# Optimization experiments

Hardware: AMD Instinct MI355X
Metric: run time of the kernel (lower is better)

Reference implementation:

```python
import jax, jax.numpy as jnp
import numpy as np

N, E, B = 50000, 800000, 64
D_IN, D_E = 192, 64
NUM_OUT = 256


def setup_inputs() -> dict:
    key = jax.random.key(0)
    ks = jax.random.split(key, 30)
    rn = lambda k, s: jax.random.normal(k, s, dtype=jnp.float32) * 0.05
    return {
        "x": jax.random.normal(ks[0], (N, D_IN), jnp.float32),
        "edge_index": jax.random.randint(ks[1], (2, E), 0, N, dtype=jnp.int32),
        "edge_attr": jax.random.normal(ks[2], (E, D_E), jnp.float32),
        "batch": jnp.sort(jax.random.randint(ks[3], (N,), 0, B, dtype=jnp.int32)),
        "W1": rn(ks[4], (D_IN, 256)), "as1": rn(ks[5], (4, 64)), "ad1": rn(ks[6], (4, 64)),
        "We1": rn(ks[7], (D_E, 256)), "ae1": rn(ks[8], (4, 64)), "b1": rn(ks[9], (256,)),
        "W2": rn(ks[10], (256, 256)), "as2": rn(ks[11], (4, 64)), "ad2": rn(ks[12], (4, 64)),
        "We2": rn(ks[13], (D_E, 256)), "ae2": rn(ks[14], (4, 64)), "b2": rn(ks[15], (256,)),
        "W3": rn(ks[16], (256, 512)), "as3": rn(ks[17], (4, 128)), "ad3": rn(ks[18], (4, 128)),
        "We3": rn(ks[19], (D_E, 512)), "ae3": rn(ks[20], (4, 128)), "b3": rn(ks[21], (128,)),
        "Wa": rn(ks[22], (128, NUM_OUT)), "ba": rn(ks[23], (NUM_OUT,)),
        "Wv": rn(ks[24], (128, 1)), "bv": rn(ks[25], (1,)),
    }


def reference(x, edge_index, edge_attr, batch,
              W1, as1, ad1, We1, ae1, b1,
              W2, as2, ad2, We2, ae2, b2,
              W3, as3, ad3, We3, ae3, b3,
              Wa, ba, Wv, bv):
    Nn = x.shape[0]
    src0, dst0 = edge_index[0], edge_index[1]
    # PyG add_self_loops(fill_value='mean'): self-loop edge_attr = mean of incoming edge_attr
    deg = jax.ops.segment_sum(jnp.ones_like(dst0, dtype=x.dtype), dst0, num_segments=Nn)
    loop_attr = jax.ops.segment_sum(edge_attr, dst0, num_segments=Nn) / jnp.maximum(deg, 1.0)[:, None]
    loop = jnp.arange(Nn, dtype=src0.dtype)
    src = jnp.concatenate([src0, loop])
    dst = jnp.concatenate([dst0, loop])
    ea = jnp.concatenate([edge_attr, loop_attr], axis=0)

    def gat(h, W, a_s, a_d, We, a_e, bias, concat):
        Hh, C = a_s.shape
        hs = (h @ W).reshape(Nn, Hh, C)                       # [N,H,C]
        al_s = (hs * a_s).sum(-1)                             # [N,H]
        al_d = (hs * a_d).sum(-1)                             # [N,H]
        al_e = ((ea @ We).reshape(-1, Hh, C) * a_e).sum(-1)   # [E+N,H]
        alpha = jax.nn.leaky_relu(al_s[src] + al_d[dst] + al_e, 0.2)
        amax = jax.ops.segment_max(alpha, dst, num_segments=Nn)
        w = jnp.exp(alpha - amax[dst])
        denom = jax.ops.segment_sum(w, dst, num_segments=Nn)
        w = w / (denom[dst] + 1e-16)                          # scatter-softmax over dst
        out = jax.ops.segment_sum(hs[src] * w[..., None], dst, num_segments=Nn)
        out = out.reshape(Nn, Hh * C) if concat else out.mean(axis=1)
        return out + bias

    h = jax.nn.relu(gat(x, W1, as1, ad1, We1, ae1, b1, True))
    h = jax.nn.relu(gat(h, W2, as2, ad2, We2, ae2, b2, True))
    h = gat(h, W3, as3, ad3, We3, ae3, b3, False)
    cnt = jax.ops.segment_sum(jnp.ones((Nn,), h.dtype), batch, num_segments=B)
    g = jax.ops.segment_sum(h, batch, num_segments=B) / jnp.maximum(cnt, 1.0)[:, None]
    logits = g @ Wa + ba
    value = g @ Wv + bv
    return jnp.concatenate([logits, value], axis=-1)  # [B, num_outputs+1]
```

## Files before the change

kernel.cpp:

```cpp
#include <hip/hip_runtime.h>
#include <hip/hip_bf16.h>


typedef __attribute__((ext_vector_type(8))) short short8;
typedef __attribute__((ext_vector_type(4))) float floatx4;

#define DEV __device__ __forceinline__

DEV unsigned short f2b(float f) {
  union { float f; unsigned u; } v; v.f = f;
  unsigned r = v.u + 0x7FFFu + ((v.u >> 16) & 1u);
  return (unsigned short)(r >> 16);
}
DEV float b2f(unsigned short u) {
  union { unsigned u; float f; } v; v.u = ((unsigned)u) << 16;
  return v.f;
}

__global__ void k_deg(const int* __restrict__ dst, int* __restrict__ deg, int E) {
  int e = blockIdx.x * 256 + threadIdx.x;
  if (e < E) atomicAdd(&deg[dst[e]], 1);
}

__global__ __launch_bounds__(1024) void k_scan(const int* __restrict__ deg,
    int* __restrict__ rowptr, int* __restrict__ cursor, int N, int E) {
  __shared__ int sd[1024];
  __shared__ int s_carry;
  int tid = threadIdx.x;
  if (tid == 0) s_carry = 0;
  __syncthreads();
  for (int base = 0; base < N; base += 8192) {
    int i0 = base + tid * 8;
    int v[8]; int s = 0;
#pragma unroll
    for (int j = 0; j < 8; j++) { int i = i0 + j; v[j] = (i < N) ? deg[i] : 0; s += v[j]; }
    int carry = s_carry;
    sd[tid] = s;
    __syncthreads();
    for (int off = 1; off < 1024; off <<= 1) {
      int t = (tid >= off) ? sd[tid - off] : 0;
      __syncthreads();
      sd[tid] += t;
      __syncthreads();
    }
    int incl = sd[tid];
    int run = carry + incl - s;
#pragma unroll
    for (int j = 0; j < 8; j++) {
      int i = i0 + j;
      if (i < N) { rowptr[i] = run; cursor[i] = run; }
      run += v[j];
    }
    __syncthreads();
    if (tid == 1023) s_carry = carry + incl;
    __syncthreads();
  }
  if (tid == 0) rowptr[N] = E;
}

__global__ void k_scatter(const int* __restrict__ src, const int* __restrict__ dst,
    int* __restrict__ cursor, int* __restrict__ csr_src, int* __restrict__ csr_eid, int E) {
  int e = blockIdx.x * 256 + threadIdx.x;
  if (e < E) {
    int d = dst[e];
    int pos = atomicAdd(&cursor[d], 1);
    csr_src[pos] = src[e];
    csr_eid[pos] = e;
  }
}

__global__ void k_wt(const float* __restrict__ W, unsigned short* __restrict__ Wt,
                     int K, int Nout) {
  int idx = blockIdx.x * 256 + threadIdx.x;
  if (idx < K * Nout) {
    int n = idx / K, k = idx - n * K;
    Wt[idx] = f2b(W[(size_t)k * Nout + n]);
  }
}

__global__ void k_wep(const float* __restrict__ We1, const float* __restrict__ ae1,
                      const float* __restrict__ We2, const float* __restrict__ ae2,
                      const float* __restrict__ We3, const float* __restrict__ ae3,
                      unsigned short* __restrict__ Wept) {
  int t = blockIdx.x * 256 + threadIdx.x;
  int j = t >> 6, c = t & 63;
  int L = j >> 2, h = j & 3;
  const float* We = (L == 0) ? We1 : (L == 1) ? We2 : We3;
  const float* ae = (L == 0) ? ae1 : (L == 1) ? ae2 : ae3;
  int C = (L == 2) ? 128 : 64;
  int HC = 4 * C;
  float s = 0.f;
  for (int cc = 0; cc < C; cc++) s += We[(size_t)c * HC + h * C + cc] * ae[h * C + cc];
  Wept[j * 64 + c] = f2b(s);
  if (t < 256) {
    int jj = 12 + (t >> 6);
    Wept[jj * 64 + (t & 63)] = 0;
  }
}

template<bool A_F32, bool OUT_F32>
__global__ __launch_bounds__(256) void k_gemm(const void* __restrict__ Ap,
    const unsigned short* __restrict__ Bt, void* __restrict__ Cp,
    int M, int Nout, int K) {
  __shared__ unsigned short As[64][40];
  __shared__ unsigned short Bs[64][40];
  const int tid = threadIdx.x;
  const int wave = tid >> 6, lane = tid & 63;
  const int quad = lane >> 4, l16 = lane & 15;
  const int m0 = blockIdx.x * 64, n0 = blockIdx.y * 64;
  const int arow = tid >> 2, acg = (tid & 3) * 8;
  floatx4 acc[4] = {{0,0,0,0},{0,0,0,0},{0,0,0,0},{0,0,0,0}};
  for (int k0 = 0; k0 < K; k0 += 32) {
    {
      int gm = m0 + arow;
      unsigned short tmp[8];
      if (A_F32) {
        const float* Af = (const float*)Ap;
        if (gm < M) {
          const float4* p = (const float4*)(Af + (size_t)gm * K + k0 + acg);
          float4 u0 = p[0], u1 = p[1];
          tmp[0]=f2b(u0.x); tmp[1]=f2b(u0.y); tmp[2]=f2b(u0.z); tmp[3]=f2b(u0.w);
          tmp[4]=f2b(u1.x); tmp[5]=f2b(u1.y); tmp[6]=f2b(u1.z); tmp[7]=f2b(u1.w);
        } else {
#pragma unroll
          for (int j = 0; j < 8; j++) tmp[j] = 0;
        }
      } else {
        const unsigned short* Ab = (const unsigned short*)Ap;
        uint4 u = {0,0,0,0};
        if (gm < M) u = *(const uint4*)(Ab + (size_t)gm * K + k0 + acg);
        *(uint4*)tmp = u;
      }
      *(uint4*)&As[arow][acg] = *(uint4*)tmp;
      int gn = n0 + arow;
      uint4 bv = {0,0,0,0};
      if (gn < Nout) bv = *(const uint4*)(Bt + (size_t)gn * K + k0 + acg);
      *(uint4*)&Bs[arow][acg] = bv;
    }
    __syncthreads();
    short8 a = *(const short8*)&As[wave * 16 + l16][quad * 8];
#pragma unroll
    for (int t = 0; t < 4; t++) {
      short8 b = *(const short8*)&Bs[t * 16 + l16][quad * 8];
      acc[t] = __builtin_amdgcn_mfma_f32_16x16x32_bf16(a, b, acc[t], 0, 0, 0);
    }
    __syncthreads();
  }
#pragma unroll
  for (int t = 0; t < 4; t++) {
#pragma unroll
    for (int r = 0; r < 4; r++) {
      int row = m0 + wave * 16 + quad * 4 + r;
      int col = n0 + t * 16 + l16;
      if (row < M && col < Nout) {
        float v = acc[t][r];
        if (OUT_F32) ((float*)Cp)[(size_t)row * Nout + col] = v;
        else ((unsigned short*)Cp)[(size_t)row * Nout + col] = f2b(v);
      }
    }
  }
}

__global__ void k_loop_ale(const int* __restrict__ rowptr, const int* __restrict__ csr_eid,
                           float* __restrict__ ale, int N, int E) {
  int n = blockIdx.x * 256 + threadIdx.x;
  if (n >= N) return;
  int s = rowptr[n], e = rowptr[n + 1];
  float a[12];
#pragma unroll
  for (int j = 0; j < 12; j++) a[j] = 0.f;
  for (int p = s; p < e; p++) {
    int eid = csr_eid[p];
    const float4* r = (const float4*)(ale + (size_t)eid * 16);
    float4 v0 = r[0], v1 = r[1], v2 = r[2];
    a[0]+=v0.x; a[1]+=v0.y; a[2]+=v0.z; a[3]+=v0.w;
    a[4]+=v1.x; a[5]+=v1.y; a[6]+=v1.z; a[7]+=v1.w;
    a[8]+=v2.x; a[9]+=v2.y; a[10]+=v2.z; a[11]+=v2.w;
  }
  float inv = 1.0f / (float)((e - s) > 1 ? (e - s) : 1);
  float* o = ale + (size_t)(E + n) * 16;
#pragma unroll
  for (int j = 0; j < 12; j++) o[j] = a[j] * inv;
  o[12] = o[13] = o[14] = o[15] = 0.f;
}

template<int VPL>
__global__ __launch_bounds__(256) void k_ald(const unsigned short* __restrict__ hs,
    const float* __restrict__ a_s, const float* __restrict__ a_d,
    float* __restrict__ als, float* __restrict__ ald, int N) {
  int node = blockIdx.x * 4 + (threadIdx.x >> 6);
  int lane = threadIdx.x & 63;
  if (node >= N) return;
  const int HC = 64 * VPL;
  const unsigned short* row = hs + (size_t)node * HC + lane * VPL;
  float vs = 0.f, vd = 0.f;
#pragma unroll
  for (int j = 0; j < VPL; j++) {
    float v = b2f(row[j]);
    vs += v * a_s[lane * VPL + j];
    vd += v * a_d[lane * VPL + j];
  }
#pragma unroll
  for (int off = 1; off < 16; off <<= 1) {
    vs += __shfl_xor(vs, off, 64);
    vd += __shfl_xor(vd, off, 64);
  }
  if ((lane & 15) == 0) {
    als[node * 4 + (lane >> 4)] = vs;
    ald[node * 4 + (lane >> 4)] = vd;
  }
}

template<int VPL, int MODE>
__global__ __launch_bounds__(256) void k_agg(const unsigned short* __restrict__ hs,
    const int* __restrict__ rowptr, const int* __restrict__ csr_src,
    const int* __restrict__ csr_eid, const float* __restrict__ ale, int L,
    const float* __restrict__ als, const float* __restrict__ ald,
    const float* __restrict__ bias, unsigned short* __restrict__ outb,
    float* __restrict__ outf, int N, int E) {
  const int HC = 64 * VPL;
  __shared__ float s_w[4][64][4];
  __shared__ int s_s[4][64];
  int wave = threadIdx.x >> 6, lane = threadIdx.x & 63;
  int node = blockIdx.x * 4 + wave;
  if (node >= N) return;
  int start = rowptr[node];
  int cnt = rowptr[node + 1] - start;
  int total = cnt + 1;
  int head = lane >> 4;
  const float4 aldv = *(const float4*)(ald + node * 4);
  float m0=-1e30f, m1=-1e30f, m2=-1e30f, m3=-1e30f;
  float d0=0.f, d1=0.f, d2=0.f, d3=0.f;
  float acc[VPL];
#pragma unroll
  for (int j = 0; j < VPL; j++) acc[j] = 0.f;
  for (int base = 0; base < total; base += 64) {
    int ei = base + lane;
    bool active = ei < total;
    float a0=-1e30f, a1=-1e30f, a2=-1e30f, a3=-1e30f;
    int sidx = node;
    if (active) {
      const float* alep;
      if (ei < cnt) {
        sidx = csr_src[start + ei];
        int eid = csr_eid[start + ei];
        alep = ale + (size_t)eid * 16 + L * 4;
      } else {
        alep = ale + (size_t)(E + node) * 16 + L * 4;
      }
      float4 ev = *(const float4*)alep;
      float4 sv = *(const float4*)(als + sidx * 4);
      a0 = sv.x + aldv.x + ev.x;
      a1 = sv.y + aldv.y + ev.y;
      a2 = sv.z + aldv.z + ev.z;
      a3 = sv.w + aldv.w + ev.w;
      a0 = a0 > 0.f ? a0 : 0.2f * a0;
      a1 = a1 > 0.f ? a1 : 0.2f * a1;
      a2 = a2 > 0.f ? a2 : 0.2f * a2;
      a3 = a3 > 0.f ? a3 : 0.2f * a3;
    }
    float c0=a0, c1=a1, c2=a2, c3=a3;
#pragma unroll
    for (int off = 32; off > 0; off >>= 1) {
      c0 = fmaxf(c0, __shfl_xor(c0, off, 64));
      c1 = fmaxf(c1, __shfl_xor(c1, off, 64));
      c2 = fmaxf(c2, __shfl_xor(c2, off, 64));
      c3 = fmaxf(c3, __shfl_xor(c3, off, 64));
    }
    float n0v = fmaxf(m0, c0), n1v = fmaxf(m1, c1), n2v = fmaxf(m2, c2), n3v = fmaxf(m3, c3);
    float p0 = active ? __expf(a0 - n0v) : 0.f;
    float p1 = active ? __expf(a1 - n1v) : 0.f;
    float p2 = active ? __expf(a2 - n2v) : 0.f;
    float p3 = active ? __expf(a3 - n3v) : 0.f;
    float s0=p0, s1=p1, s2=p2, s3=p3;
#pragma unroll
    for (int off = 32; off > 0; off >>= 1) {
      s0 += __shfl_xor(s0, off, 64);
      s1 += __shfl_xor(s1, off, 64);
      s2 += __shfl_xor(s2, off, 64);
      s3 += __shfl_xor(s3, off, 64);
    }
    float r0 = __expf(m0 - n0v), r1 = __expf(m1 - n1v);
    float r2 = __expf(m2 - n2v), r3 = __expf(m3 - n3v);
    d0 = d0 * r0 + s0; d1 = d1 * r1 + s1; d2 = d2 * r2 + s2; d3 = d3 * r3 + s3;
    float rh = head == 0 ? r0 : head == 1 ? r1 : head == 2 ? r2 : r3;
#pragma unroll
    for (int j = 0; j < VPL; j++) acc[j] *= rh;
    m0 = n0v; m1 = n1v; m2 = n2v; m3 = n3v;
    s_w[wave][lane][0] = p0; s_w[wave][lane][1] = p1;
    s_w[wave][lane][2] = p2; s_w[wave][lane][3] = p3;
    s_s[wave][lane] = sidx;
    __threadfence_block();
    int chunk = total - base; if (chunk > 64) chunk = 64;
    for (int t = 0; t < chunk; t++) {
      float w = s_w[wave][t][head];
      int sp = s_s[wave][t];
      const unsigned short* rowp = hs + (size_t)sp * HC + lane * VPL;
      if constexpr (VPL == 4) {
        ushort4 u = *(const ushort4*)rowp;
        acc[0] += w * b2f(u.x); acc[1] += w * b2f(u.y);
        acc[2] += w * b2f(u.z); acc[3] += w * b2f(u.w);
      } else {
        ushort4 u0 = ((const ushort4*)rowp)[0];
        ushort4 u1 = ((const ushort4*)rowp)[1];
        acc[0] += w * b2f(u0.x); acc[1] += w * b2f(u0.y);
        acc[2] += w * b2f(u0.z); acc[3] += w * b2f(u0.w);
        acc[4] += w * b2f(u1.x); acc[5] += w * b2f(u1.y);
        acc[6] += w * b2f(u1.z); acc[7] += w * b2f(u1.w);
      }
    }
  }
  float dh = head == 0 ? d0 : head == 1 ? d1 : head == 2 ? d2 : d3;
  float inv = 1.0f / (dh + 1e-16f);
  if constexpr (MODE == 0) {
#pragma unroll
    for (int j = 0; j < VPL; j++) {
      float v = acc[j] * inv + bias[lane * VPL + j];
      v = fmaxf(v, 0.f);
      outb[(size_t)node * HC + lane * VPL + j] = f2b(v);
    }
  } else {
#pragma unroll
    for (int j = 0; j < VPL; j++) {
      float v = acc[j] * inv;
      v += __shfl_xor(v, 16, 64);
      v += __shfl_xor(v, 32, 64);
      acc[j] = v * 0.25f;
    }
    if (lane < 16) {
#pragma unroll
      for (int j = 0; j < VPL; j++)
        outf[(size_t)node * 128 + lane * VPL + j] = acc[j] + bias[lane * VPL + j];
    }
  }
}

__global__ __launch_bounds__(256) void k_pool(const float* __restrict__ out3,
    const int* __restrict__ bat, float* __restrict__ g, int* __restrict__ cntb, int N) {
  int wid = blockIdx.x * 4 + (threadIdx.x >> 6);
  int lane = threadIdx.x & 63;
  int per = (N + 255) / 256;
  int s = wid * per, e = s + per;
  if (e > N) e = N;
  if (s >= e) return;
  int cur = bat[s];
  float ax = 0.f, ay = 0.f; int run = 0;
  for (int n = s; n < e; n++) {
    int b = bat[n];
    if (b != cur) {
      atomicAdd(&g[cur * 128 + lane * 2], ax);
      atomicAdd(&g[cur * 128 + lane * 2 + 1], ay);
      if (lane == 0) atomicAdd(&cntb[cur], run);
      ax = 0.f; ay = 0.f; run = 0; cur = b;
    }
    float2 v = *(const float2*)(out3 + (size_t)n * 128 + lane * 2);
    ax += v.x; ay += v.y; run++;
  }
  atomicAdd(&g[cur * 128 + lane * 2], ax);
  atomicAdd(&g[cur * 128 + lane * 2 + 1], ay);
  if (lane == 0) atomicAdd(&cntb[cur], run);
}

__global__ __launch_bounds__(320) void k_final(const float* __restrict__ g,
    const int* __restrict__ cntb, const float* __restrict__ Wa, const float* __restrict__ ba,
    const float* __restrict__ Wv, const float* __restrict__ bv, float* __restrict__ out) {
  __shared__ float gm[128];
  int b = blockIdx.x, t = threadIdx.x;
  if (t < 128) {
    float c = (float)cntb[b];
    gm[t] = g[b * 128 + t] / fmaxf(c, 1.f);
  }
  __syncthreads();
  if (t < 257) {
    float acc = 0.f;
    if (t < 256) {
      for (int k = 0; k < 128; k++) acc += gm[k] * Wa[k * 256 + t];
      acc += ba[t];
    } else {
      for (int k = 0; k < 128; k++) acc += gm[k] * Wv[k];
      acc += bv[0];
    }
    out[b * 257 + t] = acc;
  }
}

extern "C" void kernel_launch(void* const* d_in, const int* in_sizes, int n_in,
                              void* d_out, int out_size, void* d_ws, size_t ws_size,
                              hipStream_t stream) {
  const float* x   = (const float*)d_in[0];
  const int*   ei  = (const int*)  d_in[1];
  const float* ea  = (const float*)d_in[2];
  const int*   bat = (const int*)  d_in[3];
  const float* W1  = (const float*)d_in[4];
  const float* as1 = (const float*)d_in[5];
  const float* ad1 = (const float*)d_in[6];
  const float* We1 = (const float*)d_in[7];
  const float* ae1 = (const float*)d_in[8];
  const float* b1  = (const float*)d_in[9];
  const float* W2  = (const float*)d_in[10];
  const float* as2 = (const float*)d_in[11];
  const float* ad2 = (const float*)d_in[12];
  const float* We2 = (const float*)d_in[13];
  const float* ae2 = (const float*)d_in[14];
  const float* b2  = (const float*)d_in[15];
  const float* W3  = (const float*)d_in[16];
  const float* as3 = (const float*)d_in[17];
  const float* ad3 = (const float*)d_in[18];
  const float* We3 = (const float*)d_in[19];
  const float* ae3 = (const float*)d_in[20];
  const float* b3  = (const float*)d_in[21];
  const float* Wa  = (const float*)d_in[22];
  const float* ba  = (const float*)d_in[23];
  const float* Wv  = (const float*)d_in[24];
  const float* bv  = (const float*)d_in[25];
  (void)n_in; (void)out_size; (void)ws_size;

  const int N = in_sizes[0] / 192;
  const int E = in_sizes[1] / 2;
  const int* srcv = ei;
  const int* dstv = ei + E;

  size_t off = 0;
  auto alloc = [&](size_t bytes) -> char* {
    char* p = (char*)d_ws + off;
    off += (bytes + 255) & ~(size_t)255;
    return p;
  };
  int* deg     = (int*)alloc((size_t)N * 4);
  int* rowptr  = (int*)alloc((size_t)(N + 1) * 4);
  int* cursor  = (int*)alloc((size_t)N * 4);
  int* csr_src = (int*)alloc((size_t)E * 4);
  int* csr_eid = (int*)alloc((size_t)E * 4);
  float* ale   = (float*)alloc((size_t)(E + N) * 16 * 4);
  unsigned short* Wept = (unsigned short*)alloc(16 * 64 * 2);
  unsigned short* W1t  = (unsigned short*)alloc(256 * 192 * 2);
  unsigned short* W2t  = (unsigned short*)alloc(256 * 256 * 2);
  unsigned short* W3t  = (unsigned short*)alloc(512 * 256 * 2);
  unsigned short* hs   = (unsigned short*)alloc((size_t)N * 512 * 2);
  unsigned short* h1   = (unsigned short*)alloc((size_t)N * 256 * 2);
  unsigned short* h2   = (unsigned short*)alloc((size_t)N * 256 * 2);
  float* out3  = (float*)alloc((size_t)N * 128 * 4);
  float* als   = (float*)alloc((size_t)N * 4 * 4);
  float* ald   = (float*)alloc((size_t)N * 4 * 4);
  float* g     = (float*)alloc(64 * 128 * 4 + 64 * 4);
  int* cntb    = (int*)(g + 64 * 128);

  hipMemsetAsync(deg, 0, (size_t)N * 4, stream);
  hipMemsetAsync(g, 0, 64 * 128 * 4 + 64 * 4, stream);

  k_deg<<<(E + 255) / 256, 256, 0, stream>>>(dstv, deg, E);
  k_scan<<<1, 1024, 0, stream>>>(deg, rowptr, cursor, N, E);
  k_scatter<<<(E + 255) / 256, 256, 0, stream>>>(srcv, dstv, cursor, csr_src, csr_eid, E);
  k_wt<<<(192 * 256 + 255) / 256, 256, 0, stream>>>(W1, W1t, 192, 256);
  k_wt<<<(256 * 256 + 255) / 256, 256, 0, stream>>>(W2, W2t, 256, 256);
  k_wt<<<(256 * 512 + 255) / 256, 256, 0, stream>>>(W3, W3t, 256, 512);
  k_wep<<<3, 256, 0, stream>>>(We1, ae1, We2, ae2, We3, ae3, Wept);
  k_gemm<true, true><<<dim3((E + 63) / 64, 1), 256, 0, stream>>>(ea, Wept, ale, E, 16, 64);
  k_loop_ale<<<(N + 255) / 256, 256, 0, stream>>>(rowptr, csr_eid, ale, N, E);
  k_gemm<true, false><<<dim3((N + 63) / 64, 4), 256, 0, stream>>>(x, W1t, hs, N, 256, 192);
  k_ald<4><<<(N + 3) / 4, 256, 0, stream>>>(hs, as1, ad1, als, ald, N);
  k_agg<4, 0><<<(N + 3) / 4, 256, 0, stream>>>(hs, rowptr, csr_src, csr_eid, ale, 0, als, ald, b1, h1, nullptr, N, E);
  k_gemm<false, false><<<dim3((N + 63) / 64, 4), 256, 0, stream>>>(h1, W2t, hs, N, 256, 256);
  k_ald<4><<<(N + 3) / 4, 256, 0, stream>>>(hs, as2, ad2, als, ald, N);
  k_agg<4, 0><<<(N + 3) / 4, 256, 0, stream>>>(hs, rowptr, csr_src, csr_eid, ale, 1, als, ald, b2, h2, nullptr, N, E);
  k_gemm<false, false><<<dim3((N + 63) / 64, 8), 256, 0, stream>>>(h2, W3t, hs, N, 512, 256);
  k_ald<8><<<(N + 3) / 4, 256, 0, stream>>>(hs, as3, ad3, als, ald, N);
  k_agg<8, 1><<<(N + 3) / 4, 256, 0, stream>>>(hs, rowptr, csr_src, csr_eid, ale, 2, als, ald, b3, nullptr, out3, N, E);
  k_pool<<<64, 256, 0, stream>>>(out3, bat, g, cntb, N);
  k_final<<<64, 320, 0, stream>>>(g, cntb, Wa, ba, Wv, bv, (float*)d_out);
}
```

Measured before the change: 1.107 ms.

## Fuse attention logits into GEMM, 16-lane-per-node aggregation, parallel scan, packed CSR

The attention source and destination logits are now computed inside the GEMM epilogue with atomic adds, which removes the separate k_ald kernels. Aggregation now gives each node 16 lanes instead of a whole wave, with wider vector loads and a two-edge unroll. The single-block scan is replaced by a three-kernel multi-block scan. CSR source and edge id are packed into int2, and edge logits are stored per layer in a [L][E+N][4] layout. Costs include the atomics, extra memsets and fewer lanes per node on high-degree nodes.

```diff
diff --git a/kernel.cpp b/kernel.cpp
--- a/kernel.cpp
+++ b/kernel.cpp
@@ -22,50 +22,63 @@
   if (e < E) atomicAdd(&deg[dst[e]], 1);
 }
 
-__global__ __launch_bounds__(1024) void k_scan(const int* __restrict__ deg,
-    int* __restrict__ rowptr, int* __restrict__ cursor, int N, int E) {
-  __shared__ int sd[1024];
-  __shared__ int s_carry;
+__global__ __launch_bounds__(256) void k_scan1(const int* __restrict__ deg,
+    int* __restrict__ rowptr, int* __restrict__ bsum, int N) {
+  __shared__ int sd[256];
+  int b = blockIdx.x, tid = threadIdx.x;
+  int i0 = b * 1024 + tid * 4;
+  int v[4]; int s = 0;
+#pragma unroll
+  for (int j = 0; j < 4; j++) { int i = i0 + j; v[j] = (i < N) ? deg[i] : 0; s += v[j]; }
+  sd[tid] = s;
+  __syncthreads();
+  for (int off = 1; off < 256; off <<= 1) {
+    int t = (tid >= off) ? sd[tid - off] : 0;
+    __syncthreads();
+    sd[tid] += t;
+    __syncthreads();
+  }
+  int run = sd[tid] - s;
+#pragma unroll
+  for (int j = 0; j < 4; j++) { int i = i0 + j; if (i < N) rowptr[i] = run; run += v[j]; }
+  if (tid == 255) bsum[b] = sd[255];
+}
+
+__global__ __launch_bounds__(256) void k_scan2(int* __restrict__ bsum, int nb) {
+  __shared__ int sd[256];
   int tid = threadIdx.x;
-  if (tid == 0) s_carry = 0;
+  int v = (tid < nb) ? bsum[tid] : 0;
+  sd[tid] = v;
   __syncthreads();
-  for (int base = 0; base < N; base += 8192) {
-    int i0 = base + tid * 8;
-    int v[8]; int s = 0;
-#pragma unroll
-    for (int j = 0; j < 8; j++) { int i = i0 + j; v[j] = (i < N) ? deg[i] : 0; s += v[j]; }
-    int carry = s_carry;
-    sd[tid] = s;
+  for (int off = 1; off < 256; off <<= 1) {
+    int t = (tid >= off) ? sd[tid - off] : 0;
     __syncthreads();
-    for (int off = 1; off < 1024; off <<= 1) {
-      int t = (tid >= off) ? sd[tid - off] : 0;
-      __syncthreads();
-      sd[tid] += t;
-      __syncthreads();
-    }
-    int incl = sd[tid];
-    int run = carry + incl - s;
-#pragma unroll
-    for (int j = 0; j < 8; j++) {
-      int i = i0 + j;
-      if (i < N) { rowptr[i] = run; cursor[i] = run; }
-      run += v[j];
-    }
+    sd[tid] += t;
     __syncthreads();
-    if (tid == 1023) s_carry = carry + incl;
-    __syncthreads();
-  }
-  if (tid == 0) rowptr[N] = E;
+  }
+  if (tid < nb) bsum[tid] = sd[tid] - v;
+}
+
+__global__ __launch_bounds__(256) void k_scan3(int* __restrict__ rowptr,
+    int* __restrict__ cursor, const int* __restrict__ bsum, int N, int E) {
+  int b = blockIdx.x, tid = threadIdx.x;
+  int add = bsum[b];
+  int i0 = b * 1024 + tid * 4;
+#pragma unroll
+  for (int j = 0; j < 4; j++) {
+    int i = i0 + j;
+    if (i < N) { int r = rowptr[i] + add; rowptr[i] = r; cursor[i] = r; }
+  }
+  if (b == 0 && tid == 0) rowptr[N] = E;
 }
 
 __global__ void k_scatter(const int* __restrict__ src, const int* __restrict__ dst,
-    int* __restrict__ cursor, int* __restrict__ csr_src, int* __restrict__ csr_eid, int E) {
+    int* __restrict__ cursor, int2* __restrict__ csr, int E) {
   int e = blockIdx.x * 256 + threadIdx.x;
   if (e < E) {
     int d = dst[e];
     int pos = atomicAdd(&cursor[d], 1);
-    csr_src[pos] = src[e];
-    csr_eid[pos] = e;
+    csr[pos] = make_int2(src[e], e);
   }
 }
 
@@ -98,10 +111,12 @@
   }
 }
 
-template<bool A_F32, bool OUT_F32>
+template<bool A_F32, int OUT_MODE, bool DO_ALD>
 __global__ __launch_bounds__(256) void k_gemm(const void* __restrict__ Ap,
     const unsigned short* __restrict__ Bt, void* __restrict__ Cp,
-    int M, int Nout, int K) {
+    int M, int Nout, int K, int EN,
+    const float* __restrict__ a_s, const float* __restrict__ a_d,
+    float* __restrict__ als, float* __restrict__ ald) {
   __shared__ unsigned short As[64][40];
   __shared__ unsigned short Bs[64][40];
   const int tid = threadIdx.x;
@@ -152,101 +167,106 @@
     for (int r = 0; r < 4; r++) {
       int row = m0 + wave * 16 + quad * 4 + r;
       int col = n0 + t * 16 + l16;
-      if (row < M && col < Nout) {
+      float v = acc[t][r];
+      if (OUT_MODE == 0) {
+        if (row < M && col < Nout)
+          ((unsigned short*)Cp)[(size_t)row * Nout + col] = f2b(v);
+      } else {
+        if (row < M && col < 12)
+          ((float*)Cp)[((size_t)(col >> 2) * EN + row) * 4 + (col & 3)] = v;
+      }
+    }
+  }
+  if constexpr (DO_ALD) {
+    int h = (n0 * 4) / Nout;
+#pragma unroll
+    for (int r = 0; r < 4; r++) {
+      float ps = 0.f, pd = 0.f;
+#pragma unroll
+      for (int t = 0; t < 4; t++) {
+        int col = n0 + t * 16 + l16;
         float v = acc[t][r];
-        if (OUT_F32) ((float*)Cp)[(size_t)row * Nout + col] = v;
-        else ((unsigned short*)Cp)[(size_t)row * Nout + col] = f2b(v);
+        ps += v * a_s[col];
+        pd += v * a_d[col];
       }
-    }
-  }
-}
-
-__global__ void k_loop_ale(const int* __restrict__ rowptr, const int* __restrict__ csr_eid,
+#pragma unroll
+      for (int off = 1; off < 16; off <<= 1) {
+        ps += __shfl_xor(ps, off, 64);
+        pd += __shfl_xor(pd, off, 64);
+      }
+      int row = m0 + wave * 16 + quad * 4 + r;
+      if (l16 == 0 && row < M) {
+        atomicAdd(&als[row * 4 + h], ps);
+        atomicAdd(&ald[row * 4 + h], pd);
+      }
+    }
+  }
+}
+
+__global__ void k_loop_ale(const int* __restrict__ rowptr, const int2* __restrict__ csr,
                            float* __restrict__ ale, int N, int E) {
   int n = blockIdx.x * 256 + threadIdx.x;
   if (n >= N) return;
+  const size_t EN = (size_t)E + N;
   int s = rowptr[n], e = rowptr[n + 1];
   float a[12];
 #pragma unroll
   for (int j = 0; j < 12; j++) a[j] = 0.f;
   for (int p = s; p < e; p++) {
-    int eid = csr_eid[p];
-    const float4* r = (const float4*)(ale + (size_t)eid * 16);
-    float4 v0 = r[0], v1 = r[1], v2 = r[2];
-    a[0]+=v0.x; a[1]+=v0.y; a[2]+=v0.z; a[3]+=v0.w;
-    a[4]+=v1.x; a[5]+=v1.y; a[6]+=v1.z; a[7]+=v1.w;
-    a[8]+=v2.x; a[9]+=v2.y; a[10]+=v2.z; a[11]+=v2.w;
+    int eid = csr[p].y;
+#pragma unroll
+    for (int L = 0; L < 3; L++) {
+      float4 v = *(const float4*)(ale + (L * EN + eid) * 4);
+      a[L * 4 + 0] += v.x; a[L * 4 + 1] += v.y;
+      a[L * 4 + 2] += v.z; a[L * 4 + 3] += v.w;
+    }
   }
   float inv = 1.0f / (float)((e - s) > 1 ? (e - s) : 1);
-  float* o = ale + (size_t)(E + n) * 16;
-#pragma unroll
-  for (int j = 0; j < 12; j++) o[j] = a[j] * inv;
-  o[12] = o[13] = o[14] = o[15] = 0.f;
-}
-
-template<int VPL>
-__global__ __launch_bounds__(256) void k_ald(const unsigned short* __restrict__ hs,
-    const float* __restrict__ a_s, const float* __restrict__ a_d,
-    float* __restrict__ als, float* __restrict__ ald, int N) {
-  int node = blockIdx.x * 4 + (threadIdx.x >> 6);
-  int lane = threadIdx.x & 63;
-  if (node >= N) return;
-  const int HC = 64 * VPL;
-  const unsigned short* row = hs + (size_t)node * HC + lane * VPL;
-  float vs = 0.f, vd = 0.f;
-#pragma unroll
-  for (int j = 0; j < VPL; j++) {
-    float v = b2f(row[j]);
-    vs += v * a_s[lane * VPL + j];
-    vd += v * a_d[lane * VPL + j];
-  }
-#pragma unroll
-  for (int off = 1; off < 16; off <<= 1) {
-    vs += __shfl_xor(vs, off, 64);
-    vd += __shfl_xor(vd, off, 64);
-  }
-  if ((lane & 15) == 0) {
-    als[node * 4 + (lane >> 4)] = vs;
-    ald[node * 4 + (lane >> 4)] = vd;
-  }
+#pragma unroll
+  for (int L = 0; L < 3; L++)
+    *(float4*)(ale + (L * EN + E + n) * 4) =
+        make_float4(a[L*4+0]*inv, a[L*4+1]*inv, a[L*4+2]*inv, a[L*4+3]*inv);
 }
 
 template<int VPL, int MODE>
 __global__ __launch_bounds__(256) void k_agg(const unsigned short* __restrict__ hs,
-    const int* __restrict__ rowptr, const int* __restrict__ csr_src,
-    const int* __restrict__ csr_eid, const float* __restrict__ ale, int L,
+    const int* __restrict__ rowptr, const int2* __restrict__ csr,
+    const float* __restrict__ ale,
     const float* __restrict__ als, const float* __restrict__ ald,
     const float* __restrict__ bias, unsigned short* __restrict__ outb,
     float* __restrict__ outf, int N, int E) {
-  const int HC = 64 * VPL;
-  __shared__ float s_w[4][64][4];
-  __shared__ int s_s[4][64];
-  int wave = threadIdx.x >> 6, lane = threadIdx.x & 63;
-  int node = blockIdx.x * 4 + wave;
+  const int HC = 16 * VPL;
+  __shared__ float s_w[4][4][16][4];
+  __shared__ int   s_s[4][4][16];
+  const int wave = threadIdx.x >> 6;
+  const int lane = threadIdx.x & 63;
+  const int grp  = lane >> 4;
+  const int sl   = lane & 15;
+  const int hd   = sl >> 2;
+  const int node = blockIdx.x * 16 + wave * 4 + grp;
   if (node >= N) return;
   int start = rowptr[node];
-  int cnt = rowptr[node + 1] - start;
+  int cnt   = rowptr[node + 1] - start;
   int total = cnt + 1;
-  int head = lane >> 4;
   const float4 aldv = *(const float4*)(ald + node * 4);
   float m0=-1e30f, m1=-1e30f, m2=-1e30f, m3=-1e30f;
   float d0=0.f, d1=0.f, d2=0.f, d3=0.f;
   float acc[VPL];
 #pragma unroll
   for (int j = 0; j < VPL; j++) acc[j] = 0.f;
-  for (int base = 0; base < total; base += 64) {
-    int ei = base + lane;
+  for (int base = 0; base < total; base += 16) {
+    int ei = base + sl;
     bool active = ei < total;
     float a0=-1e30f, a1=-1e30f, a2=-1e30f, a3=-1e30f;
     int sidx = node;
     if (active) {
       const float* alep;
       if (ei < cnt) {
-        sidx = csr_src[start + ei];
-        int eid = csr_eid[start + ei];
-        alep = ale + (size_t)eid * 16 + L * 4;
+        int2 se = csr[start + ei];
+        sidx = se.x;
+        alep = ale + (size_t)se.y * 4;
       } else {
-        alep = ale + (size_t)(E + node) * 16 + L * 4;
+        alep = ale + ((size_t)E + node) * 4;
       }
       float4 ev = *(const float4*)alep;
       float4 sv = *(const float4*)(als + sidx * 4);
@@ -261,7 +281,7 @@
     }
     float c0=a0, c1=a1, c2=a2, c3=a3;
 #pragma unroll
-    for (int off = 32; off > 0; off >>= 1) {
+    for (int off = 8; off > 0; off >>= 1) {
       c0 = fmaxf(c0, __shfl_xor(c0, off, 64));
       c1 = fmaxf(c1, __shfl_xor(c1, off, 64));
       c2 = fmaxf(c2, __shfl_xor(c2, off, 64));
@@ -274,7 +294,7 @@
     float p3 = active ? __expf(a3 - n3v) : 0.f;
     float s0=p0, s1=p1, s2=p2, s3=p3;
 #pragma unroll
-    for (int off = 32; off > 0; off >>= 1) {
+    for (int off = 8; off > 0; off >>= 1) {
       s0 += __shfl_xor(s0, off, 64);
       s1 += __shfl_xor(s1, off, 64);
       s2 += __shfl_xor(s2, off, 64);
@@ -283,54 +303,64 @@
     float r0 = __expf(m0 - n0v), r1 = __expf(m1 - n1v);
     float r2 = __expf(m2 - n2v), r3 = __expf(m3 - n3v);
     d0 = d0 * r0 + s0; d1 = d1 * r1 + s1; d2 = d2 * r2 + s2; d3 = d3 * r3 + s3;
-    float rh = head == 0 ? r0 : head == 1 ? r1 : head == 2 ? r2 : r3;
+    float rh = hd == 0 ? r0 : hd == 1 ? r1 : hd == 2 ? r2 : r3;
 #pragma unroll
     for (int j = 0; j < VPL; j++) acc[j] *= rh;
     m0 = n0v; m1 = n1v; m2 = n2v; m3 = n3v;
-    s_w[wave][lane][0] = p0; s_w[wave][lane][1] = p1;
-    s_w[wave][lane][2] = p2; s_w[wave][lane][3] = p3;
-    s_s[wave][lane] = sidx;
+    *(float4*)&s_w[wave][grp][sl][0] = make_float4(p0, p1, p2, p3);
+    s_s[wave][grp][sl] = sidx;
     __threadfence_block();
-    int chunk = total - base; if (chunk > 64) chunk = 64;
-    for (int t = 0; t < chunk; t++) {
-      float w = s_w[wave][t][head];
-      int sp = s_s[wave][t];
-      const unsigned short* rowp = hs + (size_t)sp * HC + lane * VPL;
-      if constexpr (VPL == 4) {
-        ushort4 u = *(const ushort4*)rowp;
-        acc[0] += w * b2f(u.x); acc[1] += w * b2f(u.y);
-        acc[2] += w * b2f(u.z); acc[3] += w * b2f(u.w);
-      } else {
-        ushort4 u0 = ((const ushort4*)rowp)[0];
-        ushort4 u1 = ((const ushort4*)rowp)[1];
-        acc[0] += w * b2f(u0.x); acc[1] += w * b2f(u0.y);
-        acc[2] += w * b2f(u0.z); acc[3] += w * b2f(u0.w);
-        acc[4] += w * b2f(u1.x); acc[5] += w * b2f(u1.y);
-        acc[6] += w * b2f(u1.z); acc[7] += w * b2f(u1.w);
-      }
-    }
-  }
-  float dh = head == 0 ? d0 : head == 1 ? d1 : head == 2 ? d2 : d3;
+    int chunk = total - base; if (chunk > 16) chunk = 16;
+    int t = 0;
+    for (; t + 2 <= chunk; t += 2) {
+      float w0 = s_w[wave][grp][t][hd];     int sp0 = s_s[wave][grp][t];
+      float w1 = s_w[wave][grp][t + 1][hd]; int sp1 = s_s[wave][grp][t + 1];
+      const unsigned short* r0p = hs + (size_t)sp0 * HC + sl * VPL;
+      const unsigned short* r1p = hs + (size_t)sp1 * HC + sl * VPL;
+      unsigned short v0[VPL], v1[VPL];
+#pragma unroll
+      for (int q = 0; q < VPL / 8; q++) ((uint4*)v0)[q] = ((const uint4*)r0p)[q];
+#pragma unroll
+      for (int q = 0; q < VPL / 8; q++) ((uint4*)v1)[q] = ((const uint4*)r1p)[q];
+#pragma unroll
+      for (int j = 0; j < VPL; j++) acc[j] += w0 * b2f(v0[j]);
+#pragma unroll
+      for (int j = 0; j < VPL; j++) acc[j] += w1 * b2f(v1[j]);
+    }
+    if (t < chunk) {
+      float w0 = s_w[wave][grp][t][hd]; int sp0 = s_s[wave][grp][t];
+      const unsigned short* r0p = hs + (size_t)sp0 * HC + sl * VPL;
+      unsigned short v0[VPL];
+#pragma unroll
+      for (int q = 0; q < VPL / 8; q++) ((uint4*)v0)[q] = ((const uint4*)r0p)[q];
+#pragma unroll
+      for (int j = 0; j < VPL; j++) acc[j] += w0 * b2f(v0[j]);
+    }
+  }
+  float dh = hd == 0 ? d0 : hd == 1 ? d1 : hd == 2 ? d2 : d3;
   float inv = 1.0f / (dh + 1e-16f);
   if constexpr (MODE == 0) {
+    unsigned short tmp[VPL];
 #pragma unroll
     for (int j = 0; j < VPL; j++) {
-      float v = acc[j] * inv + bias[lane * VPL + j];
-      v = fmaxf(v, 0.f);
-      outb[(size_t)node * HC + lane * VPL + j] = f2b(v);
-    }
+      float v = acc[j] * inv + bias[sl * VPL + j];
+      tmp[j] = f2b(fmaxf(v, 0.f));
+    }
+    unsigned short* op = outb + (size_t)node * HC + sl * VPL;
+#pragma unroll
+    for (int q = 0; q < VPL / 8; q++) ((uint4*)op)[q] = ((uint4*)tmp)[q];
   } else {
 #pragma unroll
     for (int j = 0; j < VPL; j++) {
       float v = acc[j] * inv;
-      v += __shfl_xor(v, 16, 64);
-      v += __shfl_xor(v, 32, 64);
+      v += __shfl_xor(v, 4, 64);
+      v += __shfl_xor(v, 8, 64);
       acc[j] = v * 0.25f;
     }
-    if (lane < 16) {
-#pragma unroll
-      for (int j = 0; j < VPL; j++)
-        outf[(size_t)node * 128 + lane * VPL + j] = acc[j] + bias[lane * VPL + j];
+    if (sl < 4) {
+      float* op = outf + (size_t)node * (4 * VPL) + sl * VPL;
+#pragma unroll
+      for (int j = 0; j < VPL; j++) op[j] = acc[j] + bias[sl * VPL + j];
     }
   }
 }
@@ -417,8 +447,10 @@
 
   const int N = in_sizes[0] / 192;
   const int E = in_sizes[1] / 2;
+  const size_t EN = (size_t)E + N;
   const int* srcv = ei;
   const int* dstv = ei + E;
+  const int nb = (N + 1023) / 1024;
 
   size_t off = 0;
   auto alloc = [&](size_t bytes) -> char* {
@@ -429,9 +461,9 @@
   int* deg     = (int*)alloc((size_t)N * 4);
   int* rowptr  = (int*)alloc((size_t)(N + 1) * 4);
   int* cursor  = (int*)alloc((size_t)N * 4);
-  int* csr_src = (int*)alloc((size_t)E * 4);
-  int* csr_eid = (int*)alloc((size_t)E * 4);
-  float* ale   = (float*)alloc((size_t)(E + N) * 16 * 4);
+  int* bsum    = (int*)alloc(256 * 4);
+  int2* csr    = (int2*)alloc((size_t)E * 8);
+  float* ale   = (float*)alloc(3 * EN * 4 * 4);
   unsigned short* Wept = (unsigned short*)alloc(16 * 64 * 2);
   unsigned short* W1t  = (unsigned short*)alloc(256 * 192 * 2);
   unsigned short* W2t  = (unsigned short*)alloc(256 * 256 * 2);
@@ -440,32 +472,44 @@
   unsigned short* h1   = (unsigned short*)alloc((size_t)N * 256 * 2);
   unsigned short* h2   = (unsigned short*)alloc((size_t)N * 256 * 2);
   float* out3  = (float*)alloc((size_t)N * 128 * 4);
-  float* als   = (float*)alloc((size_t)N * 4 * 4);
-  float* ald   = (float*)alloc((size_t)N * 4 * 4);
+  float* als_all = (float*)alloc((size_t)N * 4 * 4 * 6);
   float* g     = (float*)alloc(64 * 128 * 4 + 64 * 4);
   int* cntb    = (int*)(g + 64 * 128);
+  float* als1 = als_all + (size_t)N * 4 * 0;
+  float* ald1 = als_all + (size_t)N * 4 * 1;
+  float* als2 = als_all + (size_t)N * 4 * 2;
+  float* ald2 = als_all + (size_t)N * 4 * 3;
+  float* als3 = als_all + (size_t)N * 4 * 4;
+  float* ald3 = als_all + (size_t)N * 4 * 5;
 
   hipMemsetAsync(deg, 0, (size_t)N * 4, stream);
+  hipMemsetAsync(als_all, 0, (size_t)N * 4 * 4 * 6, stream);
   hipMemsetAsync(g, 0, 64 * 128 * 4 + 64 * 4, stream);
 
   k_deg<<<(E + 255) / 256, 256, 0, stream>>>(dstv, deg, E);
-  k_scan<<<1, 1024, 0, stream>>>(deg, rowptr, cursor, N, E);
-  k_scatter<<<(E + 255) / 256, 256, 0, stream>>>(srcv, dstv, cursor, csr_src, csr_eid, E);
+  k_scan1<<<nb, 256, 0, stream>>>(deg, rowptr, bsum, N);
+  k_scan2<<<1, 256, 0, stream>>>(bsum, nb);
+  k_scan3<<<nb, 256, 0, stream>>>(rowptr, cursor, bsum, N, E);
+  k_scatter<<<(E + 255) / 256, 256, 0, stream>>>(srcv, dstv, cursor, csr, E);
   k_wt<<<(192 * 256 + 255) / 256, 256, 0, stream>>>(W1, W1t, 192, 256);
   k_wt<<<(256 * 256 + 255) / 256, 256, 0, stream>>>(W2, W2t, 256, 256);
   k_wt<<<(256 * 512 + 255) / 256, 256, 0, stream>>>(W3, W3t, 256, 512);
   k_wep<<<3, 256, 0, stream>>>(We1, ae1, We2, ae2, We3, ae3, Wept);
-  k_gemm<true, true><<<dim3((E + 63) / 64, 1), 256, 0, stream>>>(ea, Wept, ale, E, 16, 64);
-  k_loop_ale<<<(N + 255) / 256, 256, 0, stream>>>(rowptr, csr_eid, ale, N, E);
-  k_gemm<true, false><<<dim3((N + 63) / 64, 4), 256, 0, stream>>>(x, W1t, hs, N, 256, 192);
-  k_ald<4><<<(N + 3) / 4, 256, 0, stream>>>(hs, as1, ad1, als, ald, N);
-  k_agg<4, 0><<<(N + 3) / 4, 256, 0, stream>>>(hs, rowptr, csr_src, csr_eid, ale, 0, als, ald, b1, h1, nullptr, N, E);
-  k_gemm<false, false><<<dim3((N + 63) / 64, 4), 256, 0, stream>>>(h1, W2t, hs, N, 256, 256);
-  k_ald<4><<<(N + 3) / 4, 256, 0, stream>>>(hs, as2, ad2, als, ald, N);
-  k_agg<4, 0><<<(N + 3) / 4, 256, 0, stream>>>(hs, rowptr, csr_src, csr_eid, ale, 1, als, ald, b2, h2, nullptr, N, E);
-  k_gemm<false, false><<<dim3((N + 63) / 64, 8), 256, 0, stream>>>(h2, W3t, hs, N, 512, 256);
-  k_ald<8><<<(N + 3) / 4, 256, 0, stream>>>(hs, as3, ad3, als, ald, N);
-  k_agg<8, 1><<<(N + 3) / 4, 256, 0, stream>>>(hs, rowptr, csr_src, csr_eid, ale, 2, als, ald, b3, nullptr, out3, N, E);
+  k_gemm<true, 2, false><<<dim3((E + 63) / 64, 1), 256, 0, stream>>>(
+      ea, Wept, ale, E, 16, 64, (int)EN, nullptr, nullptr, nullptr, nullptr);
+  k_loop_ale<<<(N + 255) / 256, 256, 0, stream>>>(rowptr, csr, ale, N, E);
+  k_gemm<true, 0, true><<<dim3((N + 63) / 64, 4), 256, 0, stream>>>(
+      x, W1t, hs, N, 256, 192, 0, as1, ad1, als1, ald1);
+  k_agg<16, 0><<<(N + 15) / 16, 256, 0, stream>>>(
+      hs, rowptr, csr, ale + 0 * EN * 4, als1, ald1, b1, h1, nullptr, N, E);
+  k_gemm<false, 0, true><<<dim3((N + 63) / 64, 4), 256, 0, stream>>>(
+      h1, W2t, hs, N, 256, 256, 0, as2, ad2, als2, ald2);
+  k_agg<16, 0><<<(N + 15) / 16, 256, 0, stream>>>(
+      hs, rowptr, csr, ale + 1 * EN * 4, als2, ald2, b2, h2, nullptr, N, E);
+  k_gemm<false, 0, true><<<dim3((N + 63) / 64, 8), 256, 0, stream>>>(
+      h2, W3t, hs, N, 512, 256, 0, as3, ad3, als3, ald3);
+  k_agg<32, 1><<<(N + 15) / 16, 256, 0, stream>>>(
+      hs, rowptr, csr, ale + 2 * EN * 4, als3, ald3, b3, nullptr, out3, N, E);
   k_pool<<<64, 256, 0, stream>>>(out3, bat, g, cntb, N);
   k_final<<<64, 320, 0, stream>>>(g, cntb, Wa, ba, Wv, bv, (float*)d_out);
 }
```

After: 1.064 ms. 1.04x faster.
